# Kernel tuning notes

Hardware: AMD Instinct MI355X
Metric: run time of the kernel (lower is better)

Reference implementation:

```python
import jax, jax.numpy as jnp
import numpy as np

VOCAB = 50257
HIDDEN = 1024
CUTOFFS = [0, 20000, 40000, VOCAB]
N_CLUSTERS = 3
N_TOKENS = 4096


def setup_inputs() -> dict:
    key = jax.random.key(0)
    k1, k2, k3, k4 = jax.random.split(key, 4)
    x = jax.random.normal(k1, (N_TOKENS, HIDDEN), dtype=jnp.float32)
    y = jax.random.randint(k2, (N_TOKENS,), 0, VOCAB, dtype=jnp.int64)
    # nn.Linear(hidden, n_clusters, bias=False) weight: [n_clusters, hidden], init std=0.02
    W_cluster = jax.random.normal(k3, (N_CLUSTERS, HIDDEN), dtype=jnp.float32) * 0.02
    logits = jax.random.normal(k4, (HIDDEN, VOCAB), dtype=jnp.float32) * 0.02
    return {"x": x, "y": y, "W_cluster": W_cluster, "logits": logits}


def reference(x, y, W_cluster, logits):
    # cluster head: [N, n_clusters]
    cluster_ll = jax.nn.log_softmax(x @ W_cluster.T, axis=1)
    nll = jnp.zeros(y.shape, dtype=x.dtype)
    for i in range(N_CLUSTERS):  # small fixed loop over clusters
        l, r = CUTOFFS[i], CUTOFFS[i + 1]
        mask = (y >= l) & (y < r)
        # tail logits for this cluster's vocab slice: [N, r-l]
        tail_logprob = jax.nn.log_softmax(x @ logits[:, l:r], axis=1)
        t = jnp.clip(y - l, 0, r - l - 1)  # in-range for masked-out tokens
        tgt_lp = jnp.take_along_axis(tail_logprob, t[:, None], axis=1)[:, 0]
        val = -cluster_ll[:, i] - tgt_lp
        nll = jnp.where(mask, val, nll)
    return nll
```

## Files before the change

### kernel.cpp

```cpp
#include <hip/hip_runtime.h>
#include <math.h>

typedef unsigned short ushort_t;
typedef __attribute__((ext_vector_type(8))) short short8;
typedef __attribute__((ext_vector_type(4))) float floatx4;

constexpr int NT = 4096;
constexpr int H  = 1024;
constexpr int V  = 50257;
constexpr int CUT1 = 20000;
constexpr int CUT2 = 40000;

constexpr int NPAD_TOK = 4224;
constexpr int NPAD_COL = 50432;
constexpr int CT0 = 157, CT1 = 157, CT2 = 81;
constexpr int CT_TOTAL = CT0 + CT1 + CT2;
constexpr int MAX_TTILES = 32;
constexpr int CT_GROUPS = (CT_TOTAL + 7) / 8;
constexpr int MFMA_GRID = 8 * CT_GROUPS * MAX_TTILES;

constexpr int FB_TILES0 = (20000 + 63) / 64;
constexpr int FB_TILES1 = (20000 + 63) / 64;
constexpr int FB_TILES2 = (V - 40000 + 63) / 64;
constexpr int FB_TOTAL = FB_TILES0 + FB_TILES1 + FB_TILES2;

__device__ __forceinline__ ushort_t f2bf(float f) {
  unsigned int u = __float_as_uint(f);
  u = (u + 0x7FFFu + ((u >> 16) & 1u)) >> 16;
  return (ushort_t)u;
}
__device__ __forceinline__ float bf2f(ushort_t b) {
  return __uint_as_float(((unsigned int)b) << 16);
}
__device__ __forceinline__ void gl_lds16(const void* g, void* l) {
  __builtin_amdgcn_global_load_lds(
      (const __attribute__((address_space(1))) void*)g,
      (__attribute__((address_space(3))) void*)l, 16, 0, 0);
}

__global__ __launch_bounds__(1024) void setup_kernel(
    const int* __restrict__ y, int* __restrict__ offsets,
    int* __restrict__ perm, float* __restrict__ sumexp) {
  __shared__ int wcnt[16][3];
  __shared__ int wstart[16][3];
  int tid = threadIdx.x, lane = tid & 63, wid = tid >> 6;
  for (int i = tid; i < NT; i += 1024) sumexp[i] = 0.f;

  int kc[4];
  unsigned long long msk[4][3];
  int cw0 = 0, cw1 = 0, cw2 = 0;
  #pragma unroll
  for (int e = 0; e < 4; e++) {
    int v = y[tid + e * 1024];
    kc[e] = (v >= CUT1) + (v >= CUT2);
    msk[e][0] = __ballot(kc[e] == 0);
    msk[e][1] = __ballot(kc[e] == 1);
    msk[e][2] = __ballot(kc[e] == 2);
    cw0 += __popcll(msk[e][0]);
    cw1 += __popcll(msk[e][1]);
    cw2 += __popcll(msk[e][2]);
  }
  if (lane == 0) { wcnt[wid][0] = cw0; wcnt[wid][1] = cw1; wcnt[wid][2] = cw2; }
  __syncthreads();
  if (tid == 0) {
    int t0 = 0, t1 = 0, t2 = 0;
    for (int wv = 0; wv < 16; wv++) { t0 += wcnt[wv][0]; t1 += wcnt[wv][1]; t2 += wcnt[wv][2]; }
    offsets[0] = 0; offsets[1] = t0; offsets[2] = t0 + t1; offsets[3] = NT;
    int c0 = 0, c1 = t0, c2 = t0 + t1;
    for (int wv = 0; wv < 16; wv++) {
      wstart[wv][0] = c0; c0 += wcnt[wv][0];
      wstart[wv][1] = c1; c1 += wcnt[wv][1];
      wstart[wv][2] = c2; c2 += wcnt[wv][2];
    }
  }
  __syncthreads();
  int r0 = wstart[wid][0], r1 = wstart[wid][1], r2 = wstart[wid][2];
  unsigned long long below = (1ull << lane) - 1ull;
  #pragma unroll
  for (int e = 0; e < 4; e++) {
    int t = tid + e * 1024;
    int c = kc[e];
    int start = (c == 0) ? r0 : ((c == 1) ? r1 : r2);
    perm[start + __popcll(msk[e][c] & below)] = t;
    r0 += __popcll(msk[e][0]);
    r1 += __popcll(msk[e][1]);
    r2 += __popcll(msk[e][2]);
  }
}

__global__ __launch_bounds__(256) void gather_kernel(
    const float* __restrict__ x, const int* __restrict__ perm,
    ushort_t* __restrict__ xb) {
  int p = blockIdx.x;
  int src = (p < NT) ? perm[p] : -1;
  int k = threadIdx.x * 4;
  ushort4 o;
  if (src >= 0) {
    float4 v = *(const float4*)&x[(size_t)src * H + k];
    o.x = f2bf(v.x); o.y = f2bf(v.y); o.z = f2bf(v.z); o.w = f2bf(v.w);
  } else {
    o.x = 0; o.y = 0; o.z = 0; o.w = 0;
  }
  *(ushort4*)&xb[(size_t)p * H + k] = o;
}

__global__ __launch_bounds__(256) void transpose_kernel(
    const float* __restrict__ logits, ushort_t* __restrict__ lt) {
  __shared__ float ts[64][129];
  int col0 = blockIdx.x * 128, k0 = blockIdx.y * 64;
  int tid = threadIdx.x;
  #pragma unroll
  for (int e = 0; e < 8; e++) {
    int i = e * 256 + tid;
    int r = i >> 5, q = i & 31;
    int col = col0 + q * 4;
    float4 v;
    if (col + 3 < V) {
      v = *(const float4*)&logits[(size_t)(k0 + r) * V + col];
    } else {
      v.x = (col + 0 < V) ? logits[(size_t)(k0 + r) * V + col + 0] : 0.f;
      v.y = (col + 1 < V) ? logits[(size_t)(k0 + r) * V + col + 1] : 0.f;
      v.z = (col + 2 < V) ? logits[(size_t)(k0 + r) * V + col + 2] : 0.f;
      v.w = (col + 3 < V) ? logits[(size_t)(k0 + r) * V + col + 3] : 0.f;
    }
    ts[r][4 * q + 0] = v.x;
    ts[r][4 * q + 1] = v.y;
    ts[r][4 * q + 2] = v.z;
    ts[r][4 * q + 3] = v.w;
  }
  __syncthreads();
  #pragma unroll
  for (int e = 0; e < 8; e++) {
    int i = e * 256 + tid;
    int col = i >> 4, kq = i & 15;
    ushort4 o;
    o.x = f2bf(ts[4 * kq + 0][col]);
    o.y = f2bf(ts[4 * kq + 1][col]);
    o.z = f2bf(ts[4 * kq + 2][col]);
    o.w = f2bf(ts[4 * kq + 3][col]);
    *(ushort4*)&lt[(size_t)(col0 + col) * H + k0 + 4 * kq] = o;
  }
}

__global__ __launch_bounds__(256) void head_kernel(
    const float* __restrict__ x, const int* __restrict__ y,
    const float* __restrict__ Wc, const ushort_t* __restrict__ lt,
    float* __restrict__ neg_cll, float* __restrict__ z_tgt) {
  int tid = threadIdx.x;
  int lane = tid & 63;
  int token = blockIdx.x * 4 + (tid >> 6);
  int yv = y[token];
  const float* xp = x + (size_t)token * H;
  const ushort_t* lp = lt + (size_t)yv * H;
  float c0 = 0.f, c1 = 0.f, c2 = 0.f, zt = 0.f;
  #pragma unroll
  for (int j = 0; j < 16; j++) {
    int h = lane + j * 64;
    float xv = xp[h];
    c0 = fmaf(xv, Wc[h], c0);
    c1 = fmaf(xv, Wc[H + h], c1);
    c2 = fmaf(xv, Wc[2 * H + h], c2);
    zt = fmaf(xv, bf2f(lp[h]), zt);
  }
  #pragma unroll
  for (int d = 32; d; d >>= 1) {
    c0 += __shfl_down(c0, d);
    c1 += __shfl_down(c1, d);
    c2 += __shfl_down(c2, d);
    zt += __shfl_down(zt, d);
  }
  if (lane == 0) {
    float m = fmaxf(c0, fmaxf(c1, c2));
    float lse = m + logf(expf(c0 - m) + expf(c1 - m) + expf(c2 - m));
    int k = (yv >= CUT1) + (yv >= CUT2);
    float ck = (k == 0) ? c0 : ((k == 1) ? c1 : c2);
    neg_cll[token] = lse - ck;
    z_tgt[token] = zt;
  }
}

__global__ __launch_bounds__(256) void mfma_kernel(
    const ushort_t* __restrict__ xb, const ushort_t* __restrict__ lt,
    const int* __restrict__ offsets, float* __restrict__ sumexp) {
  int id = blockIdx.x;
  int xcd = id & 7;
  int j = id >> 3;
  int ct = xcd + 8 * (j >> 5);
  int tt = j & 31;
  if (ct >= CT_TOTAL) return;

  int c, col0, colEnd;
  if (ct < CT0)            { c = 0; col0 = ct * 128;                      colEnd = CUT1; }
  else if (ct < CT0 + CT1) { c = 1; col0 = CUT1 + (ct - CT0) * 128;       colEnd = CUT2; }
  else                     { c = 2; col0 = CUT2 + (ct - CT0 - CT1) * 128; colEnd = V; }

  int t0 = offsets[c] + tt * 128;
  int tEnd = offsets[c + 1];
  if (t0 >= tEnd) return;

  __shared__ __align__(16) ushort_t xs[128 * 64];
  __shared__ __align__(16) ushort_t ls[128 * 64];

  int tid = threadIdx.x;
  int lane = tid & 63;
  int w = tid >> 6;
  int wm = w >> 1, wn = w & 1;
  int m_in = lane & 15, quad = lane >> 4;

  int srow = lane >> 3;
  int sc = lane & 7;
  int gchunk = sc ^ srow;
  const ushort_t* ga[4];
  const ushort_t* gb[4];
  ushort_t* la[4];
  ushort_t* lb[4];
  #pragma unroll
  for (int cc = 0; cc < 4; cc++) {
    int r0 = w * 32 + cc * 8;
    ga[cc] = xb + (size_t)(t0 + r0 + srow) * H + gchunk * 8;
    gb[cc] = lt + (size_t)(col0 + r0 + srow) * H + gchunk * 8;
    la[cc] = &xs[r0 * 64];
    lb[cc] = &ls[r0 * 64];
  }

  floatx4 acc[4][4];
  #pragma unroll
  for (int i = 0; i < 4; i++)
    #pragma unroll
    for (int jj = 0; jj < 4; jj++)
      acc[i][jj] = (floatx4){0.f, 0.f, 0.f, 0.f};

  for (int k0 = 0; k0 < H; k0 += 64) {
    __syncthreads();
    #pragma unroll
    for (int cc = 0; cc < 4; cc++) {
      gl_lds16(ga[cc], la[cc]);
      gl_lds16(gb[cc], lb[cc]);
      ga[cc] += 64; gb[cc] += 64;
    }
    __syncthreads();

    #pragma unroll
    for (int h = 0; h < 2; h++) {
      short8 af[4], bf[4];
      #pragma unroll
      for (int i = 0; i < 4; i++) {
        int row = wm * 64 + i * 16 + m_in;
        int slot = (h * 4 + quad) ^ (row & 7);
        af[i] = *(const short8*)&xs[row * 64 + slot * 8];
      }
      #pragma unroll
      for (int jj = 0; jj < 4; jj++) {
        int row = wn * 64 + jj * 16 + m_in;
        int slot = (h * 4 + quad) ^ (row & 7);
        bf[jj] = *(const short8*)&ls[row * 64 + slot * 8];
      }
      #pragma unroll
      for (int i = 0; i < 4; i++)
        #pragma unroll
        for (int jj = 0; jj < 4; jj++)
          acc[i][jj] = __builtin_amdgcn_mfma_f32_16x16x32_bf16(af[i], bf[jj], acc[i][jj], 0, 0, 0);
    }
  }

  #pragma unroll
  for (int i = 0; i < 4; i++) {
    #pragma unroll
    for (int r = 0; r < 4; r++) {
      float s = 0.f;
      #pragma unroll
      for (int jj = 0; jj < 4; jj++) {
        int col = col0 + wn * 64 + jj * 16 + m_in;
        if (col < colEnd) s += __expf(acc[i][jj][r]);
      }
      s += __shfl_down(s, 8, 16);
      s += __shfl_down(s, 4, 16);
      s += __shfl_down(s, 2, 16);
      s += __shfl_down(s, 1, 16);
      if (m_in == 0) {
        int rowt = wm * 64 + i * 16 + quad * 4 + r;
        if (t0 + rowt < tEnd) atomicAdd(&sumexp[t0 + rowt], s);
      }
    }
  }
}

__global__ __launch_bounds__(256) void final_kernel(
    const int* __restrict__ perm, const float* __restrict__ neg_cll,
    const float* __restrict__ z_tgt, const float* __restrict__ sumexp,
    float* __restrict__ out) {
  int p = blockIdx.x * 256 + threadIdx.x;
  if (p < NT) {
    int t = perm[p];
    out[t] = neg_cll[t] + logf(sumexp[p]) - z_tgt[t];
  }
}

__global__ __launch_bounds__(256) void head_kernel_fb(
    const float* __restrict__ x, const int* __restrict__ y,
    const float* __restrict__ Wc, const float* __restrict__ logits,
    float* __restrict__ neg_cll, float* __restrict__ z_tgt) {
  int tid = threadIdx.x;
  int lane = tid & 63;
  int token = blockIdx.x * 4 + (tid >> 6);
  int yv = y[token];
  const float* xp = x + (size_t)token * H;
  float c0 = 0.f, c1 = 0.f, c2 = 0.f, zt = 0.f;
  #pragma unroll
  for (int j = 0; j < 16; j++) {
    int h = lane + j * 64;
    float xv = xp[h];
    c0 = fmaf(xv, Wc[h], c0);
    c1 = fmaf(xv, Wc[H + h], c1);
    c2 = fmaf(xv, Wc[2 * H + h], c2);
    zt = fmaf(xv, logits[(size_t)h * V + yv], zt);
  }
  #pragma unroll
  for (int d = 32; d; d >>= 1) {
    c0 += __shfl_down(c0, d);
    c1 += __shfl_down(c1, d);
    c2 += __shfl_down(c2, d);
    zt += __shfl_down(zt, d);
  }
  if (lane == 0) {
    float m = fmaxf(c0, fmaxf(c1, c2));
    float lse = m + logf(expf(c0 - m) + expf(c1 - m) + expf(c2 - m));
    int k = (yv >= CUT1) + (yv >= CUT2);
    float ck = (k == 0) ? c0 : ((k == 1) ? c1 : c2);
    neg_cll[token] = lse - ck;
    z_tgt[token] = zt;
  }
}

__global__ __launch_bounds__(256) void main_kernel_fb(
    const float* __restrict__ x, const float* __restrict__ logits,
    const int* __restrict__ offsets, const int* __restrict__ perm,
    float* __restrict__ sumexp) {
  int ct = blockIdx.x;
  int c, lct;
  if (ct < FB_TILES0)                  { c = 0; lct = ct; }
  else if (ct < FB_TILES0 + FB_TILES1) { c = 1; lct = ct - FB_TILES0; }
  else                                 { c = 2; lct = ct - FB_TILES0 - FB_TILES1; }
  int colBase = (c == 0) ? 0 : ((c == 1) ? CUT1 : CUT2);
  int colEnd  = (c == 0) ? CUT1 : ((c == 1) ? CUT2 : V);
  int col0 = colBase + lct * 64;
  int ncols = min(64, colEnd - col0);

  int t0 = offsets[c] + blockIdx.y * 64;
  int tEnd = offsets[c + 1];
  if (t0 >= tEnd) return;
  int ntok = min(64, tEnd - t0);

  __shared__ int tok_s[64];
  __shared__ float xsf[32][68];
  __shared__ float lsm[32][68];

  int tid = threadIdx.x;
  if (tid < 64) tok_s[tid] = perm[t0 + min(tid, ntok - 1)];
  __syncthreads();

  int tg = tid >> 4;
  int cg = tid & 15;
  float acc[4][4] = {};

  for (int h0 = 0; h0 < H; h0 += 32) {
    __syncthreads();
    #pragma unroll
    for (int e = 0; e < 8; e++) {
      int elem = e * 256 + tid;
      int tt = elem >> 5, kk = elem & 31;
      xsf[kk][tt] = x[(size_t)tok_s[tt] * H + h0 + kk];
    }
    #pragma unroll
    for (int e = 0; e < 8; e++) {
      int elem = e * 256 + tid;
      int kk = elem >> 6, cc = elem & 63;
      lsm[kk][cc] = (cc < ncols) ? logits[(size_t)(h0 + kk) * V + col0 + cc] : 0.f;
    }
    __syncthreads();
    #pragma unroll
    for (int kk = 0; kk < 32; kk++) {
      float4 xv = *(const float4*)&xsf[kk][4 * tg];
      float4 lv = *(const float4*)&lsm[kk][4 * cg];
      acc[0][0] = fmaf(xv.x, lv.x, acc[0][0]);
      acc[0][1] = fmaf(xv.x, lv.y, acc[0][1]);
      acc[0][2] = fmaf(xv.x, lv.z, acc[0][2]);
      acc[0][3] = fmaf(xv.x, lv.w, acc[0][3]);
      acc[1][0] = fmaf(xv.y, lv.x, acc[1][0]);
      acc[1][1] = fmaf(xv.y, lv.y, acc[1][1]);
      acc[1][2] = fmaf(xv.y, lv.z, acc[1][2]);
      acc[1][3] = fmaf(xv.y, lv.w, acc[1][3]);
      acc[2][0] = fmaf(xv.z, lv.x, acc[2][0]);
      acc[2][1] = fmaf(xv.z, lv.y, acc[2][1]);
      acc[2][2] = fmaf(xv.z, lv.z, acc[2][2]);
      acc[2][3] = fmaf(xv.z, lv.w, acc[2][3]);
      acc[3][0] = fmaf(xv.w, lv.x, acc[3][0]);
      acc[3][1] = fmaf(xv.w, lv.y, acc[3][1]);
      acc[3][2] = fmaf(xv.w, lv.z, acc[3][2]);
      acc[3][3] = fmaf(xv.w, lv.w, acc[3][3]);
    }
  }

  float s[4];
  #pragma unroll
  for (int i = 0; i < 4; i++) {
    float v = 0.f;
    #pragma unroll
    for (int j = 0; j < 4; j++) {
      if (4 * cg + j < ncols) v += expf(acc[i][j]);
    }
    s[i] = v;
  }
  #pragma unroll
  for (int i = 0; i < 4; i++) {
    #pragma unroll
    for (int d = 8; d; d >>= 1) s[i] += __shfl_down(s[i], d, 16);
  }
  if (cg == 0) {
    #pragma unroll
    for (int i = 0; i < 4; i++) {
      int tt = 4 * tg + i;
      if (tt < ntok) atomicAdd(&sumexp[tok_s[tt]], s[i]);
    }
  }
}

__global__ __launch_bounds__(256) void final_kernel_fb(
    const float* __restrict__ neg_cll, const float* __restrict__ z_tgt,
    const float* __restrict__ sumexp, float* __restrict__ out) {
  int i = blockIdx.x * 256 + threadIdx.x;
  if (i < NT) out[i] = neg_cll[i] + logf(sumexp[i]) - z_tgt[i];
}

extern "C" void kernel_launch(void* const* d_in, const int* in_sizes, int n_in,
                              void* d_out, int out_size, void* d_ws,
                              size_t ws_size, hipStream_t stream) {
  const float* x      = (const float*)d_in[0];
  const int*   y      = (const int*)d_in[1];
  const float* Wc     = (const float*)d_in[2];
  const float* logits = (const float*)d_in[3];
  float* out = (float*)d_out;

  char* ws = (char*)d_ws;
  int*   offsets = (int*)ws;
  int*   perm    = (int*)(ws + 256);
  float* sumexp  = (float*)(ws + 16896);
  float* neg_cll = (float*)(ws + 33280);
  float* z_tgt   = (float*)(ws + 49664);
  ushort_t* xb   = (ushort_t*)(ws + 66048);
  ushort_t* lt   = (ushort_t*)(ws + 66048 + (size_t)NPAD_TOK * H * 2);
  const size_t WS_NEED = 66048 + (size_t)NPAD_TOK * H * 2 + (size_t)NPAD_COL * H * 2;

  setup_kernel<<<1, 1024, 0, stream>>>(y, offsets, perm, sumexp);

  if (ws_size >= WS_NEED) {
    gather_kernel<<<NPAD_TOK, 256, 0, stream>>>(x, perm, xb);
    dim3 tg(NPAD_COL / 128, H / 64);
    transpose_kernel<<<tg, 256, 0, stream>>>(logits, lt);
    head_kernel<<<NT / 4, 256, 0, stream>>>(x, y, Wc, lt, neg_cll, z_tgt);
    mfma_kernel<<<MFMA_GRID, 256, 0, stream>>>(xb, lt, offsets, sumexp);
    final_kernel<<<NT / 256, 256, 0, stream>>>(perm, neg_cll, z_tgt, sumexp, out);
  } else {
    head_kernel_fb<<<NT / 4, 256, 0, stream>>>(x, y, Wc, logits, neg_cll, z_tgt);
    dim3 grid(FB_TOTAL, 64);
    main_kernel_fb<<<grid, 256, 0, stream>>>(x, logits, offsets, perm, sumexp);
    final_kernel_fb<<<NT / 256, 256, 0, stream>>>(neg_cll, z_tgt, sumexp, out);
  }
}
```

Before: 598.2 us.

## Double-buffer LDS staging in MFMA sumexp kernel and reduce atomics via LDS

The main MFMA kernel now double-buffers its shared-memory tiles. It issues the next K-slice's global-to-LDS loads before computing on the current one, using explicit vmcnt waits and raw barriers so that memory latency overlaps with MFMA work. It raises wave priority around the MFMA block and merges the two column-half partial sums through LDS, which halves the global atomicAdds. The transpose/convert kernel also writes 16-byte bf16 vectors instead of 8-byte ones. LDS use doubles, which may reduce occupancy.

```diff
diff --git a/kernel.cpp b/kernel.cpp
--- a/kernel.cpp
+++ b/kernel.cpp
@@ -130,15 +130,13 @@
   }
   __syncthreads();
   #pragma unroll
-  for (int e = 0; e < 8; e++) {
+  for (int e = 0; e < 4; e++) {
     int i = e * 256 + tid;
-    int col = i >> 4, kq = i & 15;
-    ushort4 o;
-    o.x = f2bf(ts[4 * kq + 0][col]);
-    o.y = f2bf(ts[4 * kq + 1][col]);
-    o.z = f2bf(ts[4 * kq + 2][col]);
-    o.w = f2bf(ts[4 * kq + 3][col]);
-    *(ushort4*)&lt[(size_t)(col0 + col) * H + k0 + 4 * kq] = o;
+    int col = i >> 3, kq8 = i & 7;
+    short8 o;
+    #pragma unroll
+    for (int d = 0; d < 8; d++) o[d] = (short)f2bf(ts[8 * kq8 + d][col]);
+    *(short8*)&lt[(size_t)(col0 + col) * H + k0 + 8 * kq8] = o;
   }
 }
 
@@ -198,8 +196,8 @@
   int tEnd = offsets[c + 1];
   if (t0 >= tEnd) return;
 
-  __shared__ __align__(16) ushort_t xs[128 * 64];
-  __shared__ __align__(16) ushort_t ls[128 * 64];
+  __shared__ __align__(16) ushort_t xs[2][128 * 64];
+  __shared__ __align__(16) ushort_t ls[2][128 * 64];
 
   int tid = threadIdx.x;
   int lane = tid & 63;
@@ -212,15 +210,13 @@
   int gchunk = sc ^ srow;
   const ushort_t* ga[4];
   const ushort_t* gb[4];
-  ushort_t* la[4];
-  ushort_t* lb[4];
+  int lofs[4];
   #pragma unroll
   for (int cc = 0; cc < 4; cc++) {
     int r0 = w * 32 + cc * 8;
     ga[cc] = xb + (size_t)(t0 + r0 + srow) * H + gchunk * 8;
     gb[cc] = lt + (size_t)(col0 + r0 + srow) * H + gchunk * 8;
-    la[cc] = &xs[r0 * 64];
-    lb[cc] = &ls[r0 * 64];
+    lofs[cc] = r0 * 64;
   }
 
   floatx4 acc[4][4];
@@ -230,16 +226,16 @@
     for (int jj = 0; jj < 4; jj++)
       acc[i][jj] = (floatx4){0.f, 0.f, 0.f, 0.f};
 
-  for (int k0 = 0; k0 < H; k0 += 64) {
-    __syncthreads();
+  auto STAGE = [&](int b) {
     #pragma unroll
     for (int cc = 0; cc < 4; cc++) {
-      gl_lds16(ga[cc], la[cc]);
-      gl_lds16(gb[cc], lb[cc]);
+      gl_lds16(ga[cc], &xs[b][lofs[cc]]);
+      gl_lds16(gb[cc], &ls[b][lofs[cc]]);
       ga[cc] += 64; gb[cc] += 64;
     }
-    __syncthreads();
-
+  };
+
+  auto COMPUTE = [&](int b) {
     #pragma unroll
     for (int h = 0; h < 2; h++) {
       short8 af[4], bf[4];
@@ -247,22 +243,47 @@
       for (int i = 0; i < 4; i++) {
         int row = wm * 64 + i * 16 + m_in;
         int slot = (h * 4 + quad) ^ (row & 7);
-        af[i] = *(const short8*)&xs[row * 64 + slot * 8];
+        af[i] = *(const short8*)&xs[b][row * 64 + slot * 8];
       }
       #pragma unroll
       for (int jj = 0; jj < 4; jj++) {
         int row = wn * 64 + jj * 16 + m_in;
         int slot = (h * 4 + quad) ^ (row & 7);
-        bf[jj] = *(const short8*)&ls[row * 64 + slot * 8];
+        bf[jj] = *(const short8*)&ls[b][row * 64 + slot * 8];
       }
+      __builtin_amdgcn_s_setprio(1);
       #pragma unroll
       for (int i = 0; i < 4; i++)
         #pragma unroll
         for (int jj = 0; jj < 4; jj++)
           acc[i][jj] = __builtin_amdgcn_mfma_f32_16x16x32_bf16(af[i], bf[jj], acc[i][jj], 0, 0, 0);
-    }
-  }
-
+      __builtin_amdgcn_s_setprio(0);
+    }
+  };
+
+  STAGE(0);
+  int cur = 0;
+  #pragma unroll
+  for (int t = 0; t < 15; ++t) {
+    STAGE(cur ^ 1);
+    asm volatile("s_waitcnt vmcnt(8)" ::: "memory");
+    __builtin_amdgcn_sched_barrier(0);
+    __builtin_amdgcn_s_barrier();
+    __builtin_amdgcn_sched_barrier(0);
+    COMPUTE(cur);
+    __builtin_amdgcn_sched_barrier(0);
+    __builtin_amdgcn_s_barrier();
+    __builtin_amdgcn_sched_barrier(0);
+    cur ^= 1;
+  }
+  asm volatile("s_waitcnt vmcnt(0)" ::: "memory");
+  __builtin_amdgcn_sched_barrier(0);
+  __builtin_amdgcn_s_barrier();
+  __builtin_amdgcn_sched_barrier(0);
+  COMPUTE(cur);
+
+  __syncthreads();
+  float* red = (float*)&xs[0][0];
   #pragma unroll
   for (int i = 0; i < 4; i++) {
     #pragma unroll
@@ -277,11 +298,14 @@
       s += __shfl_down(s, 4, 16);
       s += __shfl_down(s, 2, 16);
       s += __shfl_down(s, 1, 16);
-      if (m_in == 0) {
-        int rowt = wm * 64 + i * 16 + quad * 4 + r;
-        if (t0 + rowt < tEnd) atomicAdd(&sumexp[t0 + rowt], s);
-      }
-    }
+      if (m_in == 0) red[w * 64 + i * 16 + quad * 4 + r] = s;
+    }
+  }
+  __syncthreads();
+  if (tid < 128) {
+    int rl = tid & 63, wm2 = tid >> 6;
+    float s = red[(wm2 * 2 + 0) * 64 + rl] + red[(wm2 * 2 + 1) * 64 + rl];
+    if (t0 + tid < tEnd) atomicAdd(&sumexp[t0 + tid], s);
   }
 }
 
```

After: 560.9 us. 6.2% less time.
